# Optimization experiments

Measured on AMD Instinct MI355X. Metric: run time of the kernel, lower is better.

The kernel has to match this reference:

```python
import jax, jax.numpy as jnp
import numpy as np

HEADS = 16
D_MODEL = 1024
D_K = D_MODEL // HEADS
B, S = 2, 2048
NEG = -1000000000.0


def setup_inputs() -> dict:
    key = jax.random.key(0)
    ks = jax.random.split(key, 8)
    q = jax.random.normal(ks[0], (B, S, D_MODEL), dtype=jnp.float32)
    k = jax.random.normal(ks[1], (B, S, D_MODEL), dtype=jnp.float32)
    v = jax.random.normal(ks[2], (B, S, D_MODEL), dtype=jnp.float32)
    mask = jax.random.randint(ks[3], (B, 1, S, S), 0, 2) > 0  # True = masked
    scale = 1.0 / np.sqrt(D_MODEL)
    Wq = jax.random.normal(ks[4], (D_MODEL, D_MODEL), dtype=jnp.float32) * scale
    Wk = jax.random.normal(ks[5], (D_MODEL, D_MODEL), dtype=jnp.float32) * scale
    Wv = jax.random.normal(ks[6], (D_MODEL, D_MODEL), dtype=jnp.float32) * scale
    Wo = jax.random.normal(ks[7], (D_MODEL, D_MODEL), dtype=jnp.float32) * scale
    return {"q": q, "k": k, "v": v, "mask": mask,
            "Wq": Wq, "Wk": Wk, "Wv": Wv, "Wo": Wo}


def reference(q, k, v, mask, Wq, Wk, Wv, Wo):
    b, s, _ = q.shape
    # torch Linear: x @ W.T ; reshape to [B, H, S, d_k]
    def proj(x, W):
        return (x @ W.T).reshape(b, -1, HEADS, D_K).transpose(0, 2, 1, 3)
    qh, kh, vh = proj(q, Wq), proj(k, Wk), proj(v, Wv)
    # scaled dot-product attention; scale uses d_k (key.shape[-1] after reshape)
    att = jnp.einsum('bhqd,bhkd->bhqk', qh, kh) / jnp.sqrt(jnp.float32(D_K))
    att = jnp.where(mask, NEG, att)
    att = jax.nn.softmax(att, axis=-1)
    out = jnp.einsum('bhqk,bhkd->bhqd', att, vh)  # [B,H,S,d_k]
    out = out.transpose(0, 2, 1, 3).reshape(b, -1, D_MODEL)
    return out @ Wo.T  # dropout is identity at inference
```

## Files before the change

kernel.cpp:

```cpp
#include <hip/hip_runtime.h>

typedef unsigned short u16;
typedef unsigned int   u32;
typedef unsigned char  u8;
typedef unsigned long long u64;
typedef __attribute__((ext_vector_type(8))) short bf16x8;
typedef __attribute__((ext_vector_type(4))) float f32x4;
typedef __attribute__((ext_vector_type(16))) float f32x16;

__device__ __forceinline__ u16 f2b(float f) {
  union { float f; u32 u; } v; v.f = f;
  u32 u = v.u;
  return (u16)((u + 0x7fffu + ((u >> 16) & 1u)) >> 16);
}
__device__ __forceinline__ float b2f(u16 x) {
  union { u32 u; float f; } v; v.u = ((u32)x) << 16; return v.f;
}
__device__ __forceinline__ u32 pk2(u16 lo, u16 hi) { return (u32)lo | ((u32)hi << 16); }

__device__ __forceinline__ float fexp2(float x) { return __builtin_amdgcn_exp2f(x); }

__device__ __forceinline__ u32 cvtpk(float lo, float hi) {
  u32 r;
  asm("v_cvt_pk_bf16_f32 %0, %1, %2" : "=v"(r) : "v"(lo), "v"(hi));
  return r;
}

__device__ __forceinline__ void swap32(u32& a, u32& b) {
  asm("v_permlane32_swap_b32 %0, %1" : "+v"(a), "+v"(b));
}

__device__ __forceinline__ void glds16(const u16* g, u16* l) {
  __builtin_amdgcn_global_load_lds((const __attribute__((address_space(1))) void*)g,
                                   (__attribute__((address_space(3))) void*)l, 16, 0, 0);
}

__global__ __launch_bounds__(256) void mask_detect(const u8* __restrict__ raw,
                                                   int* __restrict__ flag) {
  int i = blockIdx.x * 256 + threadIdx.x;
  uint4 x = ((const uint4*)raw)[i];
  u32 o = x.x | x.y | x.z | x.w;
  u32 a1 = o & 0x0000ff00u;
  u32 a2 = o & 0xffff0000u;
  u64 b1 = __ballot(a1 != 0);
  u64 b2 = __ballot(a2 != 0);
  if ((threadIdx.x & 63) == 0) {
    if (b1) atomicOr(&flag[0], 1);
    if (b2) atomicOr(&flag[1], 1);
  }
}

__global__ __launch_bounds__(256) void mask_bits(const u8* __restrict__ raw,
                                                 u64* __restrict__ out,
                                                 const int* __restrict__ flag) {
  int f = flag[0] ? 2 : (flag[1] ? 1 : 0);
  int i = blockIdx.x * 256 + threadIdx.x;
  bool bit;
  if (f == 2)      bit = raw[i] != 0;
  else if (f == 0) bit = ((const int*)raw)[i] != 0;
  else             bit = ((const float*)raw)[i] != 0.0f;
  u64 b = __ballot(bit);
  if ((threadIdx.x & 63) == 0) out[i >> 6] = b;
}

__global__ __launch_bounds__(256) void conv_all(
    const float* __restrict__ W0, const float* __restrict__ W1,
    const float* __restrict__ W2, const float* __restrict__ W3,
    const float* __restrict__ A0, const float* __restrict__ A1,
    const float* __restrict__ A2,
    u16* __restrict__ o0, u16* __restrict__ o1, u16* __restrict__ o2,
    u16* __restrict__ o3, u16* __restrict__ o4, u16* __restrict__ o5,
    u16* __restrict__ o6) {
  int gid = blockIdx.x * 256 + threadIdx.x;
  const float* src; u16* dst; int off;
  if (gid < 524288) {
    int wz = gid >> 17; off = (gid & 131071) * 8;
    src = wz == 0 ? W0 : wz == 1 ? W1 : wz == 2 ? W2 : W3;
    dst = wz == 0 ? o0 : wz == 1 ? o1 : wz == 2 ? o2 : o3;
  } else {
    int g2 = gid - 524288;
    int az = g2 >> 19; off = (g2 & 524287) * 8;
    src = az == 0 ? A0 : az == 1 ? A1 : A2;
    dst = az == 0 ? o4 : az == 1 ? o5 : o6;
  }
  float4 a = *(const float4*)(src + off), b2 = *(const float4*)(src + off + 4);
  uint4 t;
  t.x = pk2(f2b(a.x), f2b(a.y));   t.y = pk2(f2b(a.z), f2b(a.w));
  t.z = pk2(f2b(b2.x), f2b(b2.y)); t.w = pk2(f2b(b2.z), f2b(b2.w));
  *(uint4*)(dst + off) = t;
}

template<int CF32>
__device__ __forceinline__ void gemm_body(
    const u16* __restrict__ Av, const u16* __restrict__ Bv, void* __restrict__ Cv,
    int N, int K, int m0, int n0, float cscale, u16* As, u16* Bs) {
  const int tid = threadIdx.x;
  const int lane = tid & 63, w = tid >> 6;
  const int lr = lane & 15, lg = lane >> 4;
  const int wm = (w >> 1) * 64, wn = (w & 1) * 64;
  const int srow = lane >> 3;
  const int selem = (((lane & 7) ^ srow) << 3);
  const int rsw = (lr & 7) << 3;

  f32x4 acc[4][4];
#pragma unroll
  for (int mi = 0; mi < 4; ++mi)
#pragma unroll
    for (int ni = 0; ni < 4; ++ni)
      acc[mi][ni] = (f32x4){0.f, 0.f, 0.f, 0.f};

#define GSTAGE(buf, k0_)                                                       \
  do {                                                                         \
    _Pragma("unroll")                                                          \
    for (int r_ = 0; r_ < 4; ++r_) {                                           \
      const int c_ = w * 4 + r_;                                               \
      const int row_ = c_ * 8 + srow;                                          \
      glds16(Av + (size_t)(m0 + row_) * K + (k0_) + selem, As + (buf) * 8192 + c_ * 512); \
      glds16(Bv + (size_t)(n0 + row_) * K + (k0_) + selem, Bs + (buf) * 8192 + c_ * 512); \
    }                                                                          \
  } while (0)

  GSTAGE(0, 0);
  __syncthreads();
  int cur = 0;
  for (int k0 = 0; k0 < K; k0 += 64) {
    if (k0 + 64 < K) GSTAGE(cur ^ 1, k0 + 64);
    bf16x8 af[4][2], bfv[4][2];
#pragma unroll
    for (int mi = 0; mi < 4; ++mi)
#pragma unroll
      for (int kk = 0; kk < 2; ++kk)
        af[mi][kk] = *(bf16x8*)&As[cur * 8192 + (wm + mi * 16 + lr) * 64 + ((kk * 32 + lg * 8) ^ rsw)];
#pragma unroll
    for (int ni = 0; ni < 4; ++ni)
#pragma unroll
      for (int kk = 0; kk < 2; ++kk)
        bfv[ni][kk] = *(bf16x8*)&Bs[cur * 8192 + (wn + ni * 16 + lr) * 64 + ((kk * 32 + lg * 8) ^ rsw)];
    __builtin_amdgcn_s_setprio(1);
#pragma unroll
    for (int mi = 0; mi < 4; ++mi)
#pragma unroll
      for (int ni = 0; ni < 4; ++ni)
#pragma unroll
        for (int kk = 0; kk < 2; ++kk)
          acc[mi][ni] = __builtin_amdgcn_mfma_f32_16x16x32_bf16(
              af[mi][kk], bfv[ni][kk], acc[mi][ni], 0, 0, 0);
    __builtin_amdgcn_s_setprio(0);
    __syncthreads();
    cur ^= 1;
  }
#undef GSTAGE
#pragma unroll
  for (int mi = 0; mi < 4; ++mi)
#pragma unroll
    for (int ni = 0; ni < 4; ++ni)
#pragma unroll
      for (int r = 0; r < 4; ++r) {
        int m = m0 + wm + mi * 16 + lg * 4 + r;
        int n = n0 + wn + ni * 16 + lr;
        float vv = acc[mi][ni][r] * cscale;
        if (CF32) ((float*)Cv)[(size_t)m * N + n] = vv;
        else      ((u16*)Cv)[(size_t)m * N + n] = f2b(vv);
      }
}

__global__ __launch_bounds__(256) void gemm_qkv(
    const u16* __restrict__ qb, const u16* __restrict__ kb, const u16* __restrict__ vb,
    const u16* __restrict__ Wqb, const u16* __restrict__ Wkb, const u16* __restrict__ Wvb,
    u16* __restrict__ Qb, u16* __restrict__ Kb, u16* __restrict__ VTb, float qscale) {
  __shared__ __align__(16) u16 As[2 * 8192];
  __shared__ __align__(16) u16 Bs[2 * 8192];
  const int z = blockIdx.z;
  const u16 *Av, *Bv; u16* Cv; int N, bxx, by; float cs = 1.0f;
  if (z < 2) {
    Av = z ? kb : qb; Bv = z ? Wkb : Wqb; Cv = z ? Kb : Qb;
    N = 1024; bxx = blockIdx.x & 7; by = blockIdx.x >> 3;
    if (!z) cs = qscale;
  } else {
    Av = Wvb; Bv = vb; Cv = VTb;
    N = 4096; bxx = blockIdx.x & 31; by = blockIdx.x >> 5;
  }
  gemm_body<0>(Av, Bv, Cv, N, 1024, by * 128, bxx * 128, cs, As, Bs);
}

__global__ __launch_bounds__(256) void gemm_o(
    const u16* __restrict__ Ob, const u16* __restrict__ Wob, float* __restrict__ C) {
  __shared__ __align__(16) u16 As[2 * 8192];
  __shared__ __align__(16) u16 Bs[2 * 8192];
  gemm_body<1>(Ob, Wob, C, 1024, 1024, blockIdx.y * 128, blockIdx.x * 128, 1.0f, As, Bs);
}

__global__ __launch_bounds__(256, 4) void flash7(const u16* __restrict__ Q,
                                                 const u16* __restrict__ K,
                                                 const u16* __restrict__ VT,
                                                 const u64* __restrict__ mpk,
                                                 u16* __restrict__ O0,
                                                 u16* __restrict__ O1,
                                                 float* __restrict__ Lp) {
  __shared__ __align__(16) u16 Ks[2][4096];
  __shared__ __align__(16) u16 Vs[2][4096];
  const int tid = threadIdx.x, lane = tid & 63, w = tid >> 6;
  const int c = lane & 31, h = lane >> 5;
  const int bid = blockIdx.x;
  const int xcd = bid & 7, idx = bid >> 3;
  const int gl = idx >> 4, qblk = idx & 15;
  const int group = xcd * 8 + gl;
  const int half = group & 1, head = (group >> 1) & 15, b = group >> 5;
  const int qw = qblk * 128 + w * 32;
  const int kt0 = half * 16;
  const size_t kbase = (size_t)b * 2048 * 1024 + (size_t)head * 64;
  const size_t vbase = (size_t)head * 64 * 4096 + (size_t)b * 2048;
  const int srow = lane >> 3;
  const int selem = (((lane & 7) ^ srow) << 3);
  const int rswc = (c & 7) << 3;

  bf16x8 qf[4];
#pragma unroll
  for (int kd = 0; kd < 4; ++kd)
    qf[kd] = *(const bf16x8*)&Q[kbase + (size_t)(qw + c) * 1024 + 16 * kd + 8 * h];

  union { u32 u[4]; bf16x8 v; } ones;
#pragma unroll
  for (int i = 0; i < 4; ++i) ones.u[i] = 0x3f803f80u;

  f32x16 accO0, accO1, accL;
#pragma unroll
  for (int i = 0; i < 16; ++i) { accO0[i] = 0.f; accO1[i] = 0.f; accL[i] = 0.f; }

  const u64* mrp = mpk + ((size_t)b * 2048 + qw + c) * 32;

#define STAGE(buf, t)                                                          \
  do {                                                                         \
    const int k0_ = (t) * 64;                                                  \
    _Pragma("unroll")                                                          \
    for (int r_ = 0; r_ < 2; ++r_) {                                           \
      const int c_ = w * 2 + r_;                                               \
      const int row_ = c_ * 8 + srow;                                          \
      glds16(K + kbase + (size_t)(k0_ + row_) * 1024 + selem, &Ks[buf][c_ * 512]); \
    }                                                                          \
    _Pragma("unroll")                                                          \
    for (int r_ = 0; r_ < 2; ++r_) {                                           \
      const int c_ = w * 2 + r_;                                               \
      const int row_ = c_ * 8 + srow;                                          \
      glds16(VT + vbase + (size_t)row_ * 4096 + k0_ + selem, &Vs[buf][c_ * 512]); \
    }                                                                          \
  } while (0)

  STAGE(0, kt0);
  u64 mb_next = mrp[kt0];
  __syncthreads();

  int cur = 0;
  for (int t = 0; t < 16; ++t) {
    const u64 mb = mb_next;
    if (t + 1 < 16) {
      STAGE(cur ^ 1, kt0 + t + 1);
      mb_next = mrp[kt0 + t + 1];
    }
    const u16* ks = Ks[cur];
    const u16* vs = Vs[cur];
    f32x16 s0, s1;
#pragma unroll
    for (int i = 0; i < 16; ++i) { s0[i] = 0.f; s1[i] = 0.f; }
    __builtin_amdgcn_s_setprio(1);
#pragma unroll
    for (int kd = 0; kd < 4; ++kd) {
      bf16x8 kf0 = *(bf16x8*)&ks[c * 64 + ((16 * kd + 8 * h) ^ rswc)];
      s0 = __builtin_amdgcn_mfma_f32_32x32x16_bf16(kf0, qf[kd], s0, 0, 0, 0);
      bf16x8 kf1 = *(bf16x8*)&ks[(32 + c) * 64 + ((16 * kd + 8 * h) ^ rswc)];
      s1 = __builtin_amdgcn_mfma_f32_32x32x16_bf16(kf1, qf[kd], s1, 0, 0, 0);
    }
    __builtin_amdgcn_s_setprio(0);
    u32 pw[2][4][2];
#pragma unroll
    for (int kb = 0; kb < 2; ++kb) {
      const u32 m32 = (u32)(mb >> (32 * kb + 4 * h));
      float pp[16];
#pragma unroll
      for (int g = 0; g < 4; ++g)
#pragma unroll
        for (int r = 0; r < 4; ++r) {
          float e = fexp2(kb == 0 ? s0[4 * g + r] : s1[4 * g + r]);
          pp[4 * g + r] = ((m32 >> (8 * g + r)) & 1) ? 0.0f : e;
        }
#pragma unroll
      for (int g = 0; g < 4; ++g)
#pragma unroll
        for (int hh = 0; hh < 2; ++hh)
          pw[kb][g][hh] = cvtpk(pp[4 * g + 2 * hh], pp[4 * g + 2 * hh + 1]);
    }
    __builtin_amdgcn_s_setprio(1);
#pragma unroll
    for (int kb = 0; kb < 2; ++kb)
#pragma unroll
      for (int s = 0; s < 2; ++s) {
        u32 w0 = pw[kb][2 * s][0], w2 = pw[kb][2 * s + 1][0];
        swap32(w0, w2);
        u32 w1 = pw[kb][2 * s][1], w3 = pw[kb][2 * s + 1][1];
        swap32(w1, w3);
        union { u32 u[4]; bf16x8 v; } af;
        af.u[0] = w0; af.u[1] = w1; af.u[2] = w2; af.u[3] = w3;
        const int ksg = kb * 2 + s;
        bf16x8 vf0 = *(bf16x8*)&vs[c * 64 + ((16 * ksg + 8 * h) ^ rswc)];
        accO0 = __builtin_amdgcn_mfma_f32_32x32x16_bf16(af.v, vf0, accO0, 0, 0, 0);
        bf16x8 vf1 = *(bf16x8*)&vs[(32 + c) * 64 + ((16 * ksg + 8 * h) ^ rswc)];
        accO1 = __builtin_amdgcn_mfma_f32_32x32x16_bf16(af.v, vf1, accO1, 0, 0, 0);
        accL  = __builtin_amdgcn_mfma_f32_32x32x16_bf16(af.v, ones.v, accL, 0, 0, 0);
      }
    __builtin_amdgcn_s_setprio(0);
    __syncthreads();
    cur ^= 1;
  }
#undef STAGE
  u16* Op = half ? O1 : O0;
  const size_t obase = (size_t)b * 2048 + qw;
#pragma unroll
  for (int g = 0; g < 4; ++g)
#pragma unroll
    for (int r = 0; r < 4; ++r) {
      const int qrow = r + 8 * g + 4 * h;
      const size_t row = obase + qrow;
      const size_t base = row * 1024 + (size_t)head * 64 + c;
      Op[base]      = f2b(accO0[4 * g + r]);
      Op[base + 32] = f2b(accO1[4 * g + r]);
      if (c == 0) Lp[(size_t)half * 65536 + row * 16 + head] = accL[4 * g + r];
    }
}

__global__ __launch_bounds__(256) void combine(const u16* __restrict__ O0,
                                               const u16* __restrict__ O1,
                                               const float* __restrict__ Lp,
                                               u16* __restrict__ Ob) {
  int gid = blockIdx.x * 256 + threadIdx.x;
  int row = gid >> 7, chb = (gid & 127) * 8;
  int head = chb >> 6;
  float l0 = Lp[(size_t)row * 16 + head];
  float l1 = Lp[65536 + (size_t)row * 16 + head];
  float inv = 1.0f / (l0 + l1);
  size_t off = (size_t)row * 1024 + chb;
  union { uint4 q; u16 s[8]; } a, b, o;
  a.q = *(const uint4*)(O0 + off);
  b.q = *(const uint4*)(O1 + off);
#pragma unroll
  for (int j = 0; j < 8; ++j)
    o.s[j] = f2b((b2f(a.s[j]) + b2f(b.s[j])) * inv);
  *(uint4*)(Ob + off) = o.q;
}

extern "C" void kernel_launch(void* const* d_in, const int* in_sizes, int n_in,
                              void* d_out, int out_size, void* d_ws, size_t ws_size,
                              hipStream_t stream) {
  const float* q    = (const float*)d_in[0];
  const float* k    = (const float*)d_in[1];
  const float* v    = (const float*)d_in[2];
  const u8*    mask = (const u8*)d_in[3];
  const float* Wq   = (const float*)d_in[4];
  const float* Wk   = (const float*)d_in[5];
  const float* Wv   = (const float*)d_in[6];
  const float* Wo   = (const float*)d_in[7];

  u8* ws = (u8*)d_ws;
  int* flag = (int*)ws;
  u64* mpk  = (u64*)(ws + 256);
  u16* Wqb  = (u16*)(ws + 256 + (1u << 20));
  u16* Wkb  = Wqb + (1 << 20);
  u16* Wvb  = Wkb + (1 << 20);
  u16* Wob  = Wvb + (1 << 20);
  const size_t NE = (size_t)4096 * 1024;
  u16* vb   = Wob + (1 << 20);
  u16* Ob   = vb;
  u16* Qb   = vb + NE;
  u16* Kb   = Qb + NE;
  u16* VTb  = Kb + NE;
  u16* qb   = (u16*)d_out;
  u16* kb   = qb + NE;
  u16* Opart0 = qb;
  u16* Opart1 = kb;
  float* Lp = (float*)Wqb;

  const float LOG2E = 1.4426950408889634f;

  hipMemsetAsync(flag, 0, 8, stream);
  mask_detect<<<32, 256, 0, stream>>>(mask, flag);
  mask_bits<<<32768, 256, 0, stream>>>(mask, mpk, flag);
  conv_all<<<8192, 256, 0, stream>>>(Wq, Wk, Wv, Wo, q, k, v,
                                     Wqb, Wkb, Wvb, Wob, qb, kb, vb);

  gemm_qkv<<<dim3(256, 1, 3), 256, 0, stream>>>(
      qb, kb, vb, Wqb, Wkb, Wvb, Qb, Kb, VTb, 0.125f * LOG2E);

  flash7<<<1024, 256, 0, stream>>>(Qb, Kb, VTb, mpk, Opart0, Opart1, Lp);
  combine<<<2048, 256, 0, stream>>>(Opart0, Opart1, Lp, Ob);

  gemm_o<<<dim3(8, 32), 256, 0, stream>>>(Ob, Wob, (float*)d_out);
}
```

Measured before the change: 161.9 us.

## Drop LDS staging in flash kernel; use single-wave blocks and VALU row sums

The flash attention kernel moves from 256-thread blocks that double-buffer K/V tiles in LDS with global_load_lds and barriers to 64-thread single-wave blocks. Each wave now loads its MFMA operands for K and V^T straight from global memory, relying on L1/L2 for reuse. The softmax denominator is now summed on the vector ALUs plus one cross-half shuffle, replacing the extra MFMA against a ones vector. This removes the barriers, the LDS footprint and a fifth of the MFMAs per tile. In exchange it loses explicit prefetch, so global-load latency is exposed each iteration, and the four waves of a query block no longer share K/V tiles.

```diff
diff --git a/kernel.cpp b/kernel.cpp
--- a/kernel.cpp
+++ b/kernel.cpp
@@ -40,10 +40,8 @@
   int i = blockIdx.x * 256 + threadIdx.x;
   uint4 x = ((const uint4*)raw)[i];
   u32 o = x.x | x.y | x.z | x.w;
-  u32 a1 = o & 0x0000ff00u;
-  u32 a2 = o & 0xffff0000u;
-  u64 b1 = __ballot(a1 != 0);
-  u64 b2 = __ballot(a2 != 0);
+  u64 b1 = __ballot((o & 0x0000ff00u) != 0);
+  u64 b2 = __ballot((o & 0xffff0000u) != 0);
   if ((threadIdx.x & 63) == 0) {
     if (b1) atomicOr(&flag[0], 1);
     if (b2) atomicOr(&flag[1], 1);
@@ -190,130 +188,96 @@
   gemm_body<1>(Ob, Wob, C, 1024, 1024, blockIdx.y * 128, blockIdx.x * 128, 1.0f, As, Bs);
 }
 
-__global__ __launch_bounds__(256, 4) void flash7(const u16* __restrict__ Q,
+__global__ __launch_bounds__(64, 4) void flash11(const u16* __restrict__ Q,
                                                  const u16* __restrict__ K,
                                                  const u16* __restrict__ VT,
                                                  const u64* __restrict__ mpk,
                                                  u16* __restrict__ O0,
                                                  u16* __restrict__ O1,
                                                  float* __restrict__ Lp) {
-  __shared__ __align__(16) u16 Ks[2][4096];
-  __shared__ __align__(16) u16 Vs[2][4096];
-  const int tid = threadIdx.x, lane = tid & 63, w = tid >> 6;
+  const int lane = threadIdx.x;
   const int c = lane & 31, h = lane >> 5;
   const int bid = blockIdx.x;
   const int xcd = bid & 7, idx = bid >> 3;
-  const int gl = idx >> 4, qblk = idx & 15;
+  const int gl = idx >> 6, sub = idx & 63;
+  const int qblk = sub >> 2, w = sub & 3;
   const int group = xcd * 8 + gl;
   const int half = group & 1, head = (group >> 1) & 15, b = group >> 5;
   const int qw = qblk * 128 + w * 32;
   const int kt0 = half * 16;
   const size_t kbase = (size_t)b * 2048 * 1024 + (size_t)head * 64;
   const size_t vbase = (size_t)head * 64 * 4096 + (size_t)b * 2048;
-  const int srow = lane >> 3;
-  const int selem = (((lane & 7) ^ srow) << 3);
-  const int rswc = (c & 7) << 3;
 
   bf16x8 qf[4];
 #pragma unroll
   for (int kd = 0; kd < 4; ++kd)
     qf[kd] = *(const bf16x8*)&Q[kbase + (size_t)(qw + c) * 1024 + 16 * kd + 8 * h];
 
-  union { u32 u[4]; bf16x8 v; } ones;
-#pragma unroll
-  for (int i = 0; i < 4; ++i) ones.u[i] = 0x3f803f80u;
-
-  f32x16 accO0, accO1, accL;
-#pragma unroll
-  for (int i = 0; i < 16; ++i) { accO0[i] = 0.f; accO1[i] = 0.f; accL[i] = 0.f; }
+  f32x16 accO0, accO1;
+#pragma unroll
+  for (int i = 0; i < 16; ++i) { accO0[i] = 0.f; accO1[i] = 0.f; }
+  float lsum = 0.f;
 
   const u64* mrp = mpk + ((size_t)b * 2048 + qw + c) * 32;
-
-#define STAGE(buf, t)                                                          \
-  do {                                                                         \
-    const int k0_ = (t) * 64;                                                  \
-    _Pragma("unroll")                                                          \
-    for (int r_ = 0; r_ < 2; ++r_) {                                           \
-      const int c_ = w * 2 + r_;                                               \
-      const int row_ = c_ * 8 + srow;                                          \
-      glds16(K + kbase + (size_t)(k0_ + row_) * 1024 + selem, &Ks[buf][c_ * 512]); \
-    }                                                                          \
-    _Pragma("unroll")                                                          \
-    for (int r_ = 0; r_ < 2; ++r_) {                                           \
-      const int c_ = w * 2 + r_;                                               \
-      const int row_ = c_ * 8 + srow;                                          \
-      glds16(VT + vbase + (size_t)row_ * 4096 + k0_ + selem, &Vs[buf][c_ * 512]); \
-    }                                                                          \
-  } while (0)
-
-  STAGE(0, kt0);
   u64 mb_next = mrp[kt0];
-  __syncthreads();
-
-  int cur = 0;
+
   for (int t = 0; t < 16; ++t) {
+    const int k0 = (kt0 + t) * 64;
     const u64 mb = mb_next;
-    if (t + 1 < 16) {
-      STAGE(cur ^ 1, kt0 + t + 1);
-      mb_next = mrp[kt0 + t + 1];
-    }
-    const u16* ks = Ks[cur];
-    const u16* vs = Vs[cur];
+    if (t + 1 < 16) mb_next = mrp[kt0 + t + 1];
+    const u16* Kt = K + kbase + (size_t)k0 * 1024;
+    const u16* Vt = VT + vbase + k0;
     f32x16 s0, s1;
 #pragma unroll
     for (int i = 0; i < 16; ++i) { s0[i] = 0.f; s1[i] = 0.f; }
     __builtin_amdgcn_s_setprio(1);
 #pragma unroll
     for (int kd = 0; kd < 4; ++kd) {
-      bf16x8 kf0 = *(bf16x8*)&ks[c * 64 + ((16 * kd + 8 * h) ^ rswc)];
+      bf16x8 kf0 = *(const bf16x8*)&Kt[(size_t)c * 1024 + 16 * kd + 8 * h];
       s0 = __builtin_amdgcn_mfma_f32_32x32x16_bf16(kf0, qf[kd], s0, 0, 0, 0);
-      bf16x8 kf1 = *(bf16x8*)&ks[(32 + c) * 64 + ((16 * kd + 8 * h) ^ rswc)];
+      bf16x8 kf1 = *(const bf16x8*)&Kt[(size_t)(32 + c) * 1024 + 16 * kd + 8 * h];
       s1 = __builtin_amdgcn_mfma_f32_32x32x16_bf16(kf1, qf[kd], s1, 0, 0, 0);
     }
     __builtin_amdgcn_s_setprio(0);
-    u32 pw[2][4][2];
 #pragma unroll
     for (int kb = 0; kb < 2; ++kb) {
       const u32 m32 = (u32)(mb >> (32 * kb + 4 * h));
-      float pp[16];
 #pragma unroll
       for (int g = 0; g < 4; ++g)
 #pragma unroll
         for (int r = 0; r < 4; ++r) {
-          float e = fexp2(kb == 0 ? s0[4 * g + r] : s1[4 * g + r]);
-          pp[4 * g + r] = ((m32 >> (8 * g + r)) & 1) ? 0.0f : e;
+          const int i = 4 * g + r;
+          float e = fexp2(kb ? s1[i] : s0[i]);
+          float pv = ((m32 >> (8 * g + r)) & 1) ? 0.0f : e;
+          if (kb) s1[i] = pv; else s0[i] = pv;
+          lsum += pv;
         }
-#pragma unroll
-      for (int g = 0; g < 4; ++g)
-#pragma unroll
-        for (int hh = 0; hh < 2; ++hh)
-          pw[kb][g][hh] = cvtpk(pp[4 * g + 2 * hh], pp[4 * g + 2 * hh + 1]);
     }
     __builtin_amdgcn_s_setprio(1);
 #pragma unroll
     for (int kb = 0; kb < 2; ++kb)
 #pragma unroll
       for (int s = 0; s < 2; ++s) {
-        u32 w0 = pw[kb][2 * s][0], w2 = pw[kb][2 * s + 1][0];
+        u32 w0 = cvtpk(kb ? s1[8 * s + 0] : s0[8 * s + 0], kb ? s1[8 * s + 1] : s0[8 * s + 1]);
+        u32 w1 = cvtpk(kb ? s1[8 * s + 2] : s0[8 * s + 2], kb ? s1[8 * s + 3] : s0[8 * s + 3]);
+        u32 w2 = cvtpk(kb ? s1[8 * s + 4] : s0[8 * s + 4], kb ? s1[8 * s + 5] : s0[8 * s + 5]);
+        u32 w3 = cvtpk(kb ? s1[8 * s + 6] : s0[8 * s + 6], kb ? s1[8 * s + 7] : s0[8 * s + 7]);
         swap32(w0, w2);
-        u32 w1 = pw[kb][2 * s][1], w3 = pw[kb][2 * s + 1][1];
         swap32(w1, w3);
         union { u32 u[4]; bf16x8 v; } af;
         af.u[0] = w0; af.u[1] = w1; af.u[2] = w2; af.u[3] = w3;
         const int ksg = kb * 2 + s;
-        bf16x8 vf0 = *(bf16x8*)&vs[c * 64 + ((16 * ksg + 8 * h) ^ rswc)];
+        bf16x8 vf0 = *(const bf16x8*)&Vt[(size_t)c * 4096 + 16 * ksg + 8 * h];
         accO0 = __builtin_amdgcn_mfma_f32_32x32x16_bf16(af.v, vf0, accO0, 0, 0, 0);
-        bf16x8 vf1 = *(bf16x8*)&vs[(32 + c) * 64 + ((16 * ksg + 8 * h) ^ rswc)];
+        bf16x8 vf1 = *(const bf16x8*)&Vt[(size_t)(32 + c) * 4096 + 16 * ksg + 8 * h];
         accO1 = __builtin_amdgcn_mfma_f32_32x32x16_bf16(af.v, vf1, accO1, 0, 0, 0);
-        accL  = __builtin_amdgcn_mfma_f32_32x32x16_bf16(af.v, ones.v, accL, 0, 0, 0);
       }
     __builtin_amdgcn_s_setprio(0);
-    __syncthreads();
-    cur ^= 1;
-  }
-#undef STAGE
+  }
+  lsum += __shfl_xor(lsum, 32);
   u16* Op = half ? O1 : O0;
   const size_t obase = (size_t)b * 2048 + qw;
+  if (h == 0) Lp[(size_t)half * 65536 + (obase + c) * 16 + head] = lsum;
 #pragma unroll
   for (int g = 0; g < 4; ++g)
 #pragma unroll
@@ -323,7 +287,6 @@
       const size_t base = row * 1024 + (size_t)head * 64 + c;
       Op[base]      = f2b(accO0[4 * g + r]);
       Op[base + 32] = f2b(accO1[4 * g + r]);
-      if (c == 0) Lp[(size_t)half * 65536 + row * 16 + head] = accL[4 * g + r];
     }
 }
 
@@ -374,8 +337,8 @@
   u16* VTb  = Kb + NE;
   u16* qb   = (u16*)d_out;
   u16* kb   = qb + NE;
-  u16* Opart0 = qb;
-  u16* Opart1 = kb;
+  u16* O0   = qb;
+  u16* O1   = kb;
   float* Lp = (float*)Wqb;
 
   const float LOG2E = 1.4426950408889634f;
@@ -389,8 +352,8 @@
   gemm_qkv<<<dim3(256, 1, 3), 256, 0, stream>>>(
       qb, kb, vb, Wqb, Wkb, Wvb, Qb, Kb, VTb, 0.125f * LOG2E);
 
-  flash7<<<1024, 256, 0, stream>>>(Qb, Kb, VTb, mpk, Opart0, Opart1, Lp);
-  combine<<<2048, 256, 0, stream>>>(Opart0, Opart1, Lp, Ob);
+  flash11<<<4096, 64, 0, stream>>>(Qb, Kb, VTb, mpk, O0, O1, Lp);
+  combine<<<2048, 256, 0, stream>>>(O0, O1, Lp, Ob);
 
   gemm_o<<<dim3(8, 32), 256, 0, stream>>>(Ob, Wob, (float*)d_out);
 }
```

New measurement: 233.3 us. 1.44x slower.
